# Optimization experiments

Measured on AMD Instinct MI355X. Metric: run time of the kernel, lower is better.

## Reference

```python
import jax, jax.numpy as jnp
import numpy as np

RES0 = 128
SCALES = [1, 2, 4, 8]
OUT_DIM = 32
PLANES = [(0, 1), (0, 2), (1, 2)]  # itertools.combinations(range(3), 2)


def _bilinear(grid, cx, cy):
    """grid: [C,H,W]; cx maps to W, cy maps to H; coords in [-1,1].
    Matches F.grid_sample(mode='bilinear', align_corners=True, padding_mode='border')."""
    C, H, W = grid.shape
    x = jnp.clip((cx + 1.0) * 0.5 * (W - 1), 0.0, W - 1)
    y = jnp.clip((cy + 1.0) * 0.5 * (H - 1), 0.0, H - 1)
    x0 = jnp.floor(x)
    y0 = jnp.floor(y)
    wx = (x - x0)[:, None]  # [N,1]
    wy = (y - y0)[:, None]
    x0i = x0.astype(jnp.int32)
    y0i = y0.astype(jnp.int32)
    x1i = jnp.minimum(x0i + 1, W - 1)
    y1i = jnp.minimum(y0i + 1, H - 1)
    g00 = grid[:, y0i, x0i].T  # [N,C]
    g01 = grid[:, y0i, x1i].T
    g10 = grid[:, y1i, x0i].T
    g11 = grid[:, y1i, x1i].T
    top = g00 * (1.0 - wx) + g01 * wx
    bot = g10 * (1.0 - wx) + g11 * wx
    return top * (1.0 - wy) + bot * wy  # [N,C]


def _interpolate_ms_features(x, ms_grids):
    feats = []
    for scale_grids in ms_grids:  # fixed 4 scales
        interp_space = 1.0
        for ci, (a, b) in enumerate(PLANES):  # fixed 3 planes
            interp_space = interp_space * _bilinear(scale_grids[ci], x[:, a], x[:, b])
        feats.append(interp_space)
    return jnp.concatenate(feats, axis=-1)  # [N, 4*OUT_DIM]


def _mlp(f, w0, w1, w2):
    h = jax.nn.relu(f @ w0)
    h = jax.nn.relu(h @ w1)
    return h @ w2  # [N,1], linear output (tcnn, bias-free)


def setup_inputs() -> dict:
    key = jax.random.key(0)
    ks = jax.random.split(key, 16)
    N = 1_000_000
    inp = {"x": jax.random.uniform(ks[0], (N, 3), jnp.float32, -1.0, 1.0)}
    i = 1
    for s, mult in enumerate(SCALES):
        R = RES0 * mult
        for p in range(3):
            # nn.init.uniform_(a=0.1, b=0.5)
            inp[f"g{s}p{p}"] = jax.random.uniform(ks[i], (OUT_DIM, R, R), jnp.float32, 0.1, 0.5)
            i += 1
    F = OUT_DIM * len(SCALES)
    inp["w0"] = jax.random.normal(ks[13], (F, 64), jnp.float32) / np.sqrt(F).astype(np.float32)
    inp["w1"] = jax.random.normal(ks[14], (64, 64), jnp.float32) / 8.0
    inp["w2"] = jax.random.normal(ks[15], (64, 1), jnp.float32) / 8.0
    return inp


def reference(x, g0p0, g0p1, g0p2, g1p0, g1p1, g1p2, g2p0, g2p1, g2p2,
              g3p0, g3p1, g3p2, w0, w1, w2):
    ms_grids = [(g0p0, g0p1, g0p2), (g1p0, g1p1, g1p2),
                (g2p0, g2p1, g2p2), (g3p0, g3p1, g3p2)]
    features = _interpolate_ms_features(x, ms_grids)
    return _mlp(features, w0, w1, w2)
```

## Files before the change

kernel.cpp:

```cpp
#include <hip/hip_runtime.h>
#include <cstddef>


typedef unsigned short ushort_t;
typedef unsigned int uint_t;
typedef __bf16 bf16x8 __attribute__((ext_vector_type(8)));
typedef float f32x4 __attribute__((ext_vector_type(4)));

struct KParams {
  const float* x;
  const void* g[12];
  const float* w0;
  const float* w1;
  const float* w2;
  const ushort_t* w0T;
  const ushort_t* w1T;
  float* out;
  int N;
};

__device__ __forceinline__ ushort_t f32_to_bf16_rne(float f) {
  uint_t u = __float_as_uint(f);
  u = (u + 0x7FFFu + ((u >> 16) & 1u)) >> 16;
  return (ushort_t)u;
}

__global__ __launch_bounds__(256) void transpose_chw_hwc_bf16(
    const float* __restrict__ in, ushort_t* __restrict__ out, int RR) {
  __shared__ float tile[32][65];
  const int p0 = blockIdx.x * 64;
  {
    const int tp = threadIdx.x & 63;
    const int tc = threadIdx.x >> 6;
#pragma unroll
    for (int cc = 0; cc < 8; ++cc) {
      const int c = cc * 4 + tc;
      tile[c][tp] = in[(size_t)c * RR + p0 + tp];
    }
  }
  __syncthreads();
  {
    const int c2 = threadIdx.x & 15;
    const int tq = threadIdx.x >> 4;
    uint_t* o32 = (uint_t*)out;
#pragma unroll
    for (int pp = 0; pp < 4; ++pp) {
      const int pos = pp * 16 + tq;
      const uint_t lo = f32_to_bf16_rne(tile[2 * c2 + 0][pos]);
      const uint_t hi = f32_to_bf16_rne(tile[2 * c2 + 1][pos]);
      o32[(size_t)(p0 + pos) * 16 + c2] = lo | (hi << 16);
    }
  }
}

__global__ __launch_bounds__(256) void prep_weights(
    const float* __restrict__ w0, const float* __restrict__ w1,
    ushort_t* __restrict__ w0T, ushort_t* __restrict__ w1T) {
  const int t = threadIdx.x;
  for (int i = t; i < 128 * 64; i += 256) {
    const int k = i >> 6, n = i & 63;
    w0T[n * 128 + k] = f32_to_bf16_rne(w0[i]);
  }
  for (int i = t; i < 64 * 64; i += 256) {
    const int k = i >> 6, n = i & 63;
    w1T[n * 64 + k] = f32_to_bf16_rne(w1[i]);
  }
}

__global__ __launch_bounds__(512, 8) void kplanes_fused_mfma(KParams P) {
  __shared__ ushort_t lds_feat[64 * 128];
  __shared__ ushort_t lds_h[64 * 64];
  __shared__ float oparts[2][64];

  const int t = threadIdx.x;
  const int blk0 = blockIdx.x * 64;

  const int pg = t >> 3;
  const int sub = t & 7;
  int Pi = blk0 + pg;
  if (Pi >= P.N) Pi = P.N - 1;
  const float c0 = P.x[3 * Pi + 0];
  const float c1 = P.x[3 * Pi + 1];
  const float c2 = P.x[3 * Pi + 2];

  float feat[4][4];
#pragma unroll
  for (int s = 0; s < 4; ++s)
#pragma unroll
    for (int c = 0; c < 4; ++c) feat[s][c] = 1.0f;

#pragma unroll
  for (int s = 0; s < 4; ++s) {
    const int R = 128 << s;
#pragma unroll
    for (int pl = 0; pl < 3; ++pl) {
      const float cx = (pl == 2) ? c1 : c0;
      const float cy = (pl == 0) ? c1 : c2;
      const float Rm1 = (float)(R - 1);
      const float u = fminf(fmaxf((cx + 1.0f) * 0.5f * Rm1, 0.0f), Rm1);
      const float v = fminf(fmaxf((cy + 1.0f) * 0.5f * Rm1, 0.0f), Rm1);
      const float fx0 = floorf(u), fy0 = floorf(v);
      const float wx = u - fx0, wy = v - fy0;
      const int x0 = (int)fx0, y0 = (int)fy0;
      const int x1 = min(x0 + 1, R - 1), y1 = min(y0 + 1, R - 1);
      const float w11 = wx * wy;
      const float w10 = wy - w11;
      const float w01 = wx - w11;
      const float w00 = 1.0f - wx - w10;

      const ushort_t* gp = (const ushort_t*)P.g[s * 3 + pl];
      const uint2 qa = *(const uint2*)(gp + (size_t)(y0 * R + x0) * 32 + sub * 4);
      const uint2 qb = *(const uint2*)(gp + (size_t)(y0 * R + x1) * 32 + sub * 4);
      const uint2 qc = *(const uint2*)(gp + (size_t)(y1 * R + x0) * 32 + sub * 4);
      const uint2 qd = *(const uint2*)(gp + (size_t)(y1 * R + x1) * 32 + sub * 4);
      float r;
      r = __uint_as_float(qd.x << 16) * w11;
      r = fmaf(__uint_as_float(qc.x << 16), w10, r);
      r = fmaf(__uint_as_float(qb.x << 16), w01, r);
      r = fmaf(__uint_as_float(qa.x << 16), w00, r);
      feat[s][0] *= r;
      r = __uint_as_float(qd.x & 0xFFFF0000u) * w11;
      r = fmaf(__uint_as_float(qc.x & 0xFFFF0000u), w10, r);
      r = fmaf(__uint_as_float(qb.x & 0xFFFF0000u), w01, r);
      r = fmaf(__uint_as_float(qa.x & 0xFFFF0000u), w00, r);
      feat[s][1] *= r;
      r = __uint_as_float(qd.y << 16) * w11;
      r = fmaf(__uint_as_float(qc.y << 16), w10, r);
      r = fmaf(__uint_as_float(qb.y << 16), w01, r);
      r = fmaf(__uint_as_float(qa.y << 16), w00, r);
      feat[s][2] *= r;
      r = __uint_as_float(qd.y & 0xFFFF0000u) * w11;
      r = fmaf(__uint_as_float(qc.y & 0xFFFF0000u), w10, r);
      r = fmaf(__uint_as_float(qb.y & 0xFFFF0000u), w01, r);
      r = fmaf(__uint_as_float(qa.y & 0xFFFF0000u), w00, r);
      feat[s][3] *= r;
    }
  }

  {
    uint_t* prow = (uint_t*)lds_feat + pg * 64;
    const int wxor = (pg & 7) << 2;
#pragma unroll
    for (int s = 0; s < 4; ++s) {
      uint_t d0, d1;
      asm("v_cvt_pk_bf16_f32 %0, %1, %2" : "=v"(d0) : "v"(feat[s][0]), "v"(feat[s][1]));
      asm("v_cvt_pk_bf16_f32 %0, %1, %2" : "=v"(d1) : "v"(feat[s][2]), "v"(feat[s][3]));
      const int idx = (s * 16 + sub * 2) ^ wxor;
      prow[idx] = d0;
      prow[idx + 1] = d1;
    }
  }
  __syncthreads();

  const int w = __builtin_amdgcn_readfirstlane(t >> 6);
  const int mt = w & 3;
  const int nt0 = (w >> 2) << 1;
  const int ln = t & 15;
  const int lq = (t >> 4) & 3;
  const int arow = mt * 16 + ln;

  const uint_t* farow = (const uint_t*)lds_feat + arow * 64;
  const int axor = (arow & 7) << 2;
  f32x4 acc0a = {0.f, 0.f, 0.f, 0.f}, acc0b = {0.f, 0.f, 0.f, 0.f};
  const ushort_t* w0a = P.w0T + (nt0 * 16 + ln) * 128 + lq * 8;
  const ushort_t* w0b = w0a + 16 * 128;
#pragma unroll
  for (int kt = 0; kt < 4; ++kt) {
    const bf16x8 aF = *(const bf16x8*)(farow + ((kt * 16 + lq * 4) ^ axor));
    const bf16x8 bFa = *(const bf16x8*)(w0a + kt * 32);
    const bf16x8 bFb = *(const bf16x8*)(w0b + kt * 32);
    acc0a = __builtin_amdgcn_mfma_f32_16x16x32_bf16(aF, bFa, acc0a, 0, 0, 0);
    acc0b = __builtin_amdgcn_mfma_f32_16x16x32_bf16(aF, bFb, acc0b, 0, 0, 0);
  }

#pragma unroll
  for (int i = 0; i < 2; ++i) {
    const f32x4 a = i ? acc0b : acc0a;
    const int col = (nt0 + i) * 16 + ln;
#pragma unroll
    for (int j = 0; j < 4; ++j) {
      const float v = fmaxf(a[j], 0.0f);
      uint_t dv;
      asm("v_cvt_pk_bf16_f32 %0, %1, %2" : "=v"(dv) : "v"(v), "v"(v));
      const int r = mt * 16 + lq * 4 + j;
      lds_h[r * 64 + (col ^ ((r & 7) << 3))] = (ushort_t)dv;
    }
  }
  __syncthreads();

  const ushort_t* hrow = lds_h + arow * 64;
  const int hxor = (arow & 7) << 3;
  f32x4 acc1a = {0.f, 0.f, 0.f, 0.f}, acc1b = {0.f, 0.f, 0.f, 0.f};
  const ushort_t* w1a = P.w1T + (nt0 * 16 + ln) * 64 + lq * 8;
  const ushort_t* w1b = w1a + 16 * 64;
#pragma unroll
  for (int kt = 0; kt < 2; ++kt) {
    const bf16x8 aF = *(const bf16x8*)(hrow + ((kt * 32 + lq * 8) ^ hxor));
    const bf16x8 bFa = *(const bf16x8*)(w1a + kt * 32);
    const bf16x8 bFb = *(const bf16x8*)(w1b + kt * 32);
    acc1a = __builtin_amdgcn_mfma_f32_16x16x32_bf16(aF, bFa, acc1a, 0, 0, 0);
    acc1b = __builtin_amdgcn_mfma_f32_16x16x32_bf16(aF, bFb, acc1b, 0, 0, 0);
  }

  const float w2a = P.w2[nt0 * 16 + ln];
  const float w2b = P.w2[(nt0 + 1) * 16 + ln];
  float part[4];
#pragma unroll
  for (int j = 0; j < 4; ++j)
    part[j] = fmaxf(acc1a[j], 0.f) * w2a + fmaxf(acc1b[j], 0.f) * w2b;
#pragma unroll
  for (int j = 0; j < 4; ++j) {
    part[j] += __shfl_xor(part[j], 1);
    part[j] += __shfl_xor(part[j], 2);
    part[j] += __shfl_xor(part[j], 4);
    part[j] += __shfl_xor(part[j], 8);
  }
  if (ln == 0) {
#pragma unroll
    for (int j = 0; j < 4; ++j)
      oparts[w >> 2][mt * 16 + lq * 4 + j] = part[j];
  }
  __syncthreads();

  if (t < 64) {
    const int Po = blk0 + t;
    if (Po < P.N) P.out[Po] = oparts[0][t] + oparts[1][t];
  }
}

__global__ __launch_bounds__(512, 8) void kplanes_fused_scalar(KParams P) {
  __shared__ float fl[64][130];
  const int t = threadIdx.x;
  const int pg = t >> 3;
  const int sub = t & 7;
  const int blk0 = blockIdx.x * 64;

  int Pi = blk0 + pg;
  if (Pi >= P.N) Pi = P.N - 1;
  const float c0 = P.x[3 * Pi + 0];
  const float c1 = P.x[3 * Pi + 1];
  const float c2 = P.x[3 * Pi + 2];

  float feat[4][4];
#pragma unroll
  for (int s = 0; s < 4; ++s)
#pragma unroll
    for (int c = 0; c < 4; ++c) feat[s][c] = 1.0f;

#pragma unroll
  for (int s = 0; s < 4; ++s) {
    const int R = 128 << s;
    const int RR = R * R;
#pragma unroll
    for (int pl = 0; pl < 3; ++pl) {
      const float cx = (pl == 2) ? c1 : c0;
      const float cy = (pl == 0) ? c1 : c2;
      const float Rm1 = (float)(R - 1);
      const float u = fminf(fmaxf((cx + 1.0f) * 0.5f * Rm1, 0.0f), Rm1);
      const float v = fminf(fmaxf((cy + 1.0f) * 0.5f * Rm1, 0.0f), Rm1);
      const float fx0 = floorf(u), fy0 = floorf(v);
      const float wx = u - fx0, wy = v - fy0;
      const int x0 = (int)fx0, y0 = (int)fy0;
      const int x1 = min(x0 + 1, R - 1), y1 = min(y0 + 1, R - 1);
      const float w11 = wx * wy;
      const float w10 = wy - w11;
      const float w01 = wx - w11;
      const float w00 = 1.0f - wx - w10;
      const float* gp = (const float*)P.g[s * 3 + pl];
      const int i00 = y0 * R + x0, i01 = y0 * R + x1;
      const int i10 = y1 * R + x0, i11 = y1 * R + x1;
#pragma unroll
      for (int c = 0; c < 4; ++c) {
        const size_t cb = (size_t)(sub * 4 + c) * RR;
        feat[s][c] *= gp[cb + i00] * w00 + gp[cb + i01] * w01 +
                      gp[cb + i10] * w10 + gp[cb + i11] * w11;
      }
    }
  }

#pragma unroll
  for (int s = 0; s < 4; ++s)
#pragma unroll
    for (int c = 0; c < 4; ++c)
      fl[pg][s * 32 + sub * 4 + c] = feat[s][c];
  __syncthreads();

  const int p = t & 63;
  const int g = __builtin_amdgcn_readfirstlane(t >> 6);

  const float* w0c = P.w0 + g * 8;
  float part[8];
#pragma unroll
  for (int jj = 0; jj < 8; ++jj) part[jj] = 0.0f;
#pragma unroll 16
  for (int k = 0; k < 128; ++k) {
    const float f = fl[p][k];
#pragma unroll
    for (int jj = 0; jj < 8; ++jj)
      part[jj] = fmaf(f, w0c[(size_t)k * 64 + jj], part[jj]);
  }
  __syncthreads();
#pragma unroll
  for (int jj = 0; jj < 8; ++jj)
    fl[p][g * 8 + jj] = fmaxf(part[jj], 0.0f);
  __syncthreads();

  const float* w1c = P.w1 + g * 8;
  float h1[8];
#pragma unroll
  for (int jj = 0; jj < 8; ++jj) h1[jj] = 0.0f;
#pragma unroll 16
  for (int k = 0; k < 64; ++k) {
    const float a = fl[p][k];
#pragma unroll
    for (int jj = 0; jj < 8; ++jj)
      h1[jj] = fmaf(a, w1c[(size_t)k * 64 + jj], h1[jj]);
  }

  const float* w2c = P.w2 + g * 8;
  float o = 0.0f;
#pragma unroll
  for (int jj = 0; jj < 8; ++jj)
    o = fmaf(fmaxf(h1[jj], 0.0f), w2c[jj], o);

  __syncthreads();
  ((float*)fl)[g * 64 + p] = o;
  __syncthreads();

  if (t < 64) {
    const int Po = blk0 + t;
    if (Po < P.N) {
      const float* f0 = (const float*)fl;
      float r = 0.0f;
#pragma unroll
      for (int j = 0; j < 8; ++j) r += f0[j * 64 + t];
      P.out[Po] = r;
    }
  }
}

extern "C" void kernel_launch(void* const* d_in, const int* in_sizes, int n_in,
                              void* d_out, int out_size, void* d_ws, size_t ws_size,
                              hipStream_t stream) {
  KParams P;
  P.x = (const float*)d_in[0];
  P.w0 = (const float*)d_in[13];
  P.w1 = (const float*)d_in[14];
  P.w2 = (const float*)d_in[15];
  P.out = (float*)d_out;
  const int N = in_sizes[0] / 3;
  P.N = N;

  size_t need = 0;
  for (int s = 0; s < 4; ++s) {
    const size_t R = (size_t)(128 << s);
    need += 3ull * 32ull * R * R * sizeof(ushort_t);
  }
  const size_t walign = (need + 255) & ~(size_t)255;
  const size_t wbytes = (size_t)(64 * 128 + 64 * 64) * sizeof(ushort_t);

  const int nblk = (N + 63) / 64;
  if (ws_size >= walign + wbytes) {
    ushort_t* w = (ushort_t*)d_ws;
    size_t off = 0;
    for (int s = 0; s < 4; ++s) {
      const int R = 128 << s;
      const int RR = R * R;
      for (int pl = 0; pl < 3; ++pl) {
        const float* src = (const float*)d_in[1 + s * 3 + pl];
        transpose_chw_hwc_bf16<<<RR / 64, 256, 0, stream>>>(src, w + off, RR);
        P.g[s * 3 + pl] = w + off;
        off += (size_t)32 * RR;
      }
    }
    ushort_t* w0T = (ushort_t*)((char*)d_ws + walign);
    ushort_t* w1T = w0T + 64 * 128;
    P.w0T = w0T;
    P.w1T = w1T;
    prep_weights<<<1, 256, 0, stream>>>(P.w0, P.w1, w0T, w1T);
    kplanes_fused_mfma<<<nblk, 512, 0, stream>>>(P);
  } else {
    for (int k = 0; k < 12; ++k) P.g[k] = (const void*)d_in[1 + k];
    P.w0T = nullptr;
    P.w1T = nullptr;
    kplanes_fused_scalar<<<nblk, 512, 0, stream>>>(P);
  }
}
```

Baseline: 764.3 us.

## Precompute bilinear indices in LDS and widen gathers to 16-byte loads

The fused kernel now computes the bilinear corner offsets and fractional weights once per point, plane and scale, spreading the 768 tasks across the block and storing them in a shared LDS arena. Each thread then reads 16-byte bf16 vectors covering 8 channels for two scales, instead of 8-byte loads for 4 channels across all four scales. This aims to cut redundant coordinate math and halve the number of gather instructions. It also merges the three per-scale transpose launches into one launch with a 3-plane grid and reuses LDS between stages. In exchange it adds an extra barrier and an LDS round-trip for the coordinates.

```diff
diff --git a/kernel.cpp b/kernel.cpp
--- a/kernel.cpp
+++ b/kernel.cpp
@@ -19,23 +19,31 @@
   int N;
 };
 
+struct TP3 {
+  const float* src[3];
+  ushort_t* dst[3];
+  int RR;
+};
+
 __device__ __forceinline__ ushort_t f32_to_bf16_rne(float f) {
   uint_t u = __float_as_uint(f);
   u = (u + 0x7FFFu + ((u >> 16) & 1u)) >> 16;
   return (ushort_t)u;
 }
 
-__global__ __launch_bounds__(256) void transpose_chw_hwc_bf16(
-    const float* __restrict__ in, ushort_t* __restrict__ out, int RR) {
+__global__ __launch_bounds__(256) void transpose3(TP3 tp) {
+  const float* __restrict__ in = tp.src[blockIdx.y];
+  ushort_t* __restrict__ out = tp.dst[blockIdx.y];
+  const int RR = tp.RR;
   __shared__ float tile[32][65];
   const int p0 = blockIdx.x * 64;
   {
-    const int tp = threadIdx.x & 63;
+    const int tp_ = threadIdx.x & 63;
     const int tc = threadIdx.x >> 6;
 #pragma unroll
     for (int cc = 0; cc < 8; ++cc) {
       const int c = cc * 4 + tc;
-      tile[c][tp] = in[(size_t)c * RR + p0 + tp];
+      tile[c][tp_] = in[(size_t)c * RR + p0 + tp_];
     }
   }
   __syncthreads();
@@ -68,89 +76,110 @@
 }
 
 __global__ __launch_bounds__(512, 8) void kplanes_fused_mfma(KParams P) {
-  __shared__ ushort_t lds_feat[64 * 128];
-  __shared__ ushort_t lds_h[64 * 64];
-  __shared__ float oparts[2][64];
+  __shared__ float arena[10240];
+  int* ci = (int*)arena;
+  float* cf = arena;
+  uint_t* feat32 = (uint_t*)(arena + 6144);
+  float* px = arena + 6144;
 
   const int t = threadIdx.x;
   const int blk0 = blockIdx.x * 64;
 
-  const int pg = t >> 3;
-  const int sub = t & 7;
-  int Pi = blk0 + pg;
-  if (Pi >= P.N) Pi = P.N - 1;
-  const float c0 = P.x[3 * Pi + 0];
-  const float c1 = P.x[3 * Pi + 1];
-  const float c2 = P.x[3 * Pi + 2];
-
-  float feat[4][4];
-#pragma unroll
-  for (int s = 0; s < 4; ++s)
-#pragma unroll
-    for (int c = 0; c < 4; ++c) feat[s][c] = 1.0f;
-
-#pragma unroll
-  for (int s = 0; s < 4; ++s) {
+  if (t < 192) {
+    const int p = t / 3, e = t - p * 3;
+    int Pi = blk0 + p;
+    if (Pi >= P.N) Pi = P.N - 1;
+    px[t] = P.x[3 * Pi + e];
+  }
+  __syncthreads();
+
+  for (int task = t; task < 768; task += 512) {
+    const int pt = task & 63;
+    const int sm = task >> 6;
+    const int pl = sm >> 2;
+    const int s = sm & 3;
+    const float cx = (pl == 2) ? px[pt * 3 + 1] : px[pt * 3 + 0];
+    const float cy = (pl == 0) ? px[pt * 3 + 1] : px[pt * 3 + 2];
     const int R = 128 << s;
+    const float Rm1 = (float)(R - 1);
+    const float u = fminf(fmaxf((cx + 1.0f) * 0.5f * Rm1, 0.0f), Rm1);
+    const float v = fminf(fmaxf((cy + 1.0f) * 0.5f * Rm1, 0.0f), Rm1);
+    const float fx0 = floorf(u), fy0 = floorf(v);
+    const int x0 = (int)fx0, y0 = (int)fy0;
+    const int x1 = min(x0 + 1, R - 1), y1 = min(y0 + 1, R - 1);
+    const int base = task * 8;
+    int4 o4;
+    o4.x = y0 * R + x0;
+    o4.y = y0 * R + x1;
+    o4.z = y1 * R + x0;
+    o4.w = y1 * R + x1;
+    *(int4*)(ci + base) = o4;
+    cf[base + 4] = u - fx0;
+    cf[base + 5] = v - fy0;
+  }
+  __syncthreads();
+
+  const int pt = t >> 3;
+  const int q = t & 7;
+  const int cg = q & 3;
+  const int sh = q >> 2;
+  uint_t* prow = feat32 + pt * 64;
+  const int wxor = (pt & 7) << 2;
+
+#pragma unroll
+  for (int j = 0; j < 2; ++j) {
+    const int s = 2 * j + sh;
+    float f[8];
+#pragma unroll
+    for (int c = 0; c < 8; ++c) f[c] = 1.0f;
+
 #pragma unroll
     for (int pl = 0; pl < 3; ++pl) {
-      const float cx = (pl == 2) ? c1 : c0;
-      const float cy = (pl == 0) ? c1 : c2;
-      const float Rm1 = (float)(R - 1);
-      const float u = fminf(fmaxf((cx + 1.0f) * 0.5f * Rm1, 0.0f), Rm1);
-      const float v = fminf(fmaxf((cy + 1.0f) * 0.5f * Rm1, 0.0f), Rm1);
-      const float fx0 = floorf(u), fy0 = floorf(v);
-      const float wx = u - fx0, wy = v - fy0;
-      const int x0 = (int)fx0, y0 = (int)fy0;
-      const int x1 = min(x0 + 1, R - 1), y1 = min(y0 + 1, R - 1);
+      const int base = ((pl * 4 + s) * 64 + pt) * 8;
+      const int4 o4 = *(const int4*)(ci + base);
+      const float wx = cf[base + 4], wy = cf[base + 5];
       const float w11 = wx * wy;
       const float w10 = wy - w11;
       const float w01 = wx - w11;
       const float w00 = 1.0f - wx - w10;
-
       const ushort_t* gp = (const ushort_t*)P.g[s * 3 + pl];
-      const uint2 qa = *(const uint2*)(gp + (size_t)(y0 * R + x0) * 32 + sub * 4);
-      const uint2 qb = *(const uint2*)(gp + (size_t)(y0 * R + x1) * 32 + sub * 4);
-      const uint2 qc = *(const uint2*)(gp + (size_t)(y1 * R + x0) * 32 + sub * 4);
-      const uint2 qd = *(const uint2*)(gp + (size_t)(y1 * R + x1) * 32 + sub * 4);
-      float r;
-      r = __uint_as_float(qd.x << 16) * w11;
-      r = fmaf(__uint_as_float(qc.x << 16), w10, r);
-      r = fmaf(__uint_as_float(qb.x << 16), w01, r);
-      r = fmaf(__uint_as_float(qa.x << 16), w00, r);
-      feat[s][0] *= r;
-      r = __uint_as_float(qd.x & 0xFFFF0000u) * w11;
-      r = fmaf(__uint_as_float(qc.x & 0xFFFF0000u), w10, r);
-      r = fmaf(__uint_as_float(qb.x & 0xFFFF0000u), w01, r);
-      r = fmaf(__uint_as_float(qa.x & 0xFFFF0000u), w00, r);
-      feat[s][1] *= r;
-      r = __uint_as_float(qd.y << 16) * w11;
-      r = fmaf(__uint_as_float(qc.y << 16), w10, r);
-      r = fmaf(__uint_as_float(qb.y << 16), w01, r);
-      r = fmaf(__uint_as_float(qa.y << 16), w00, r);
-      feat[s][2] *= r;
-      r = __uint_as_float(qd.y & 0xFFFF0000u) * w11;
-      r = fmaf(__uint_as_float(qc.y & 0xFFFF0000u), w10, r);
-      r = fmaf(__uint_as_float(qb.y & 0xFFFF0000u), w01, r);
-      r = fmaf(__uint_as_float(qa.y & 0xFFFF0000u), w00, r);
-      feat[s][3] *= r;
-    }
-  }
-
-  {
-    uint_t* prow = (uint_t*)lds_feat + pg * 64;
-    const int wxor = (pg & 7) << 2;
-#pragma unroll
-    for (int s = 0; s < 4; ++s) {
-      uint_t d0, d1;
-      asm("v_cvt_pk_bf16_f32 %0, %1, %2" : "=v"(d0) : "v"(feat[s][0]), "v"(feat[s][1]));
-      asm("v_cvt_pk_bf16_f32 %0, %1, %2" : "=v"(d1) : "v"(feat[s][2]), "v"(feat[s][3]));
-      const int idx = (s * 16 + sub * 2) ^ wxor;
-      prow[idx] = d0;
-      prow[idx + 1] = d1;
-    }
-  }
-  __syncthreads();
+      const uint4 qa = *(const uint4*)(gp + (size_t)o4.x * 32 + cg * 8);
+      const uint4 qb = *(const uint4*)(gp + (size_t)o4.y * 32 + cg * 8);
+      const uint4 qc = *(const uint4*)(gp + (size_t)o4.z * 32 + cg * 8);
+      const uint4 qd = *(const uint4*)(gp + (size_t)o4.w * 32 + cg * 8);
+#define CH2(dA, dB, dC, dD, i0, i1)                                \
+  {                                                                \
+    float rl = __uint_as_float((dD) << 16) * w11;                  \
+    rl = fmaf(__uint_as_float((dC) << 16), w10, rl);               \
+    rl = fmaf(__uint_as_float((dB) << 16), w01, rl);               \
+    rl = fmaf(__uint_as_float((dA) << 16), w00, rl);               \
+    f[i0] *= rl;                                                   \
+    float rh = __uint_as_float((dD)&0xFFFF0000u) * w11;            \
+    rh = fmaf(__uint_as_float((dC)&0xFFFF0000u), w10, rh);         \
+    rh = fmaf(__uint_as_float((dB)&0xFFFF0000u), w01, rh);         \
+    rh = fmaf(__uint_as_float((dA)&0xFFFF0000u), w00, rh);         \
+    f[i1] *= rh;                                                   \
+  }
+      CH2(qa.x, qb.x, qc.x, qd.x, 0, 1)
+      CH2(qa.y, qb.y, qc.y, qd.y, 2, 3)
+      CH2(qa.z, qb.z, qc.z, qd.z, 4, 5)
+      CH2(qa.w, qb.w, qc.w, qd.w, 6, 7)
+#undef CH2
+    }
+
+    uint_t d0, d1, d2, d3;
+    asm("v_cvt_pk_bf16_f32 %0, %1, %2" : "=v"(d0) : "v"(f[0]), "v"(f[1]));
+    asm("v_cvt_pk_bf16_f32 %0, %1, %2" : "=v"(d1) : "v"(f[2]), "v"(f[3]));
+    asm("v_cvt_pk_bf16_f32 %0, %1, %2" : "=v"(d2) : "v"(f[4]), "v"(f[5]));
+    asm("v_cvt_pk_bf16_f32 %0, %1, %2" : "=v"(d3) : "v"(f[6]), "v"(f[7]));
+    uint4 dv;
+    dv.x = d0; dv.y = d1; dv.z = d2; dv.w = d3;
+    *(uint4*)(prow + ((s * 16 + cg * 4) ^ wxor)) = dv;
+  }
+  __syncthreads();
+
+  ushort_t* lds_h = (ushort_t*)arena;
+  float(*oparts)[64] = (float(*)[64])(arena + 2048);
 
   const int w = __builtin_amdgcn_readfirstlane(t >> 6);
   const int mt = w & 3;
@@ -159,7 +188,7 @@
   const int lq = (t >> 4) & 3;
   const int arow = mt * 16 + ln;
 
-  const uint_t* farow = (const uint_t*)lds_feat + arow * 64;
+  const uint_t* farow = feat32 + arow * 64;
   const int axor = (arow & 7) << 2;
   f32x4 acc0a = {0.f, 0.f, 0.f, 0.f}, acc0b = {0.f, 0.f, 0.f, 0.f};
   const ushort_t* w0a = P.w0T + (nt0 * 16 + ln) * 128 + lq * 8;
@@ -178,11 +207,11 @@
     const f32x4 a = i ? acc0b : acc0a;
     const int col = (nt0 + i) * 16 + ln;
 #pragma unroll
-    for (int j = 0; j < 4; ++j) {
-      const float v = fmaxf(a[j], 0.0f);
+    for (int jj = 0; jj < 4; ++jj) {
+      const float v = fmaxf(a[jj], 0.0f);
       uint_t dv;
       asm("v_cvt_pk_bf16_f32 %0, %1, %2" : "=v"(dv) : "v"(v), "v"(v));
-      const int r = mt * 16 + lq * 4 + j;
+      const int r = mt * 16 + lq * 4 + jj;
       lds_h[r * 64 + (col ^ ((r & 7) << 3))] = (ushort_t)dv;
     }
   }
@@ -206,19 +235,19 @@
   const float w2b = P.w2[(nt0 + 1) * 16 + ln];
   float part[4];
 #pragma unroll
-  for (int j = 0; j < 4; ++j)
-    part[j] = fmaxf(acc1a[j], 0.f) * w2a + fmaxf(acc1b[j], 0.f) * w2b;
-#pragma unroll
-  for (int j = 0; j < 4; ++j) {
-    part[j] += __shfl_xor(part[j], 1);
-    part[j] += __shfl_xor(part[j], 2);
-    part[j] += __shfl_xor(part[j], 4);
-    part[j] += __shfl_xor(part[j], 8);
+  for (int jj = 0; jj < 4; ++jj)
+    part[jj] = fmaxf(acc1a[jj], 0.f) * w2a + fmaxf(acc1b[jj], 0.f) * w2b;
+#pragma unroll
+  for (int jj = 0; jj < 4; ++jj) {
+    part[jj] += __shfl_xor(part[jj], 1);
+    part[jj] += __shfl_xor(part[jj], 2);
+    part[jj] += __shfl_xor(part[jj], 4);
+    part[jj] += __shfl_xor(part[jj], 8);
   }
   if (ln == 0) {
 #pragma unroll
-    for (int j = 0; j < 4; ++j)
-      oparts[w >> 2][mt * 16 + lq * 4 + j] = part[j];
+    for (int jj = 0; jj < 4; ++jj)
+      oparts[w >> 2][mt * 16 + lq * 4 + jj] = part[jj];
   }
   __syncthreads();
 
@@ -366,12 +395,16 @@
     for (int s = 0; s < 4; ++s) {
       const int R = 128 << s;
       const int RR = R * R;
+      TP3 tp;
+      tp.RR = RR;
       for (int pl = 0; pl < 3; ++pl) {
-        const float* src = (const float*)d_in[1 + s * 3 + pl];
-        transpose_chw_hwc_bf16<<<RR / 64, 256, 0, stream>>>(src, w + off, RR);
+        tp.src[pl] = (const float*)d_in[1 + s * 3 + pl];
+        tp.dst[pl] = w + off;
         P.g[s * 3 + pl] = w + off;
         off += (size_t)32 * RR;
       }
+      dim3 grid(RR / 64, 3);
+      transpose3<<<grid, 256, 0, stream>>>(tp);
     }
     ushort_t* w0T = (ushort_t*)((char*)d_ws + walign);
     ushort_t* w1T = w0T + 64 * 128;
```

Result: faster. 730.0 us (-4.5%).
